# Optimization experiments

Hardware: AMD Instinct MI355X
Metric: run time of the kernel (lower is better)

## Reference

```python
import jax, jax.numpy as jnp
import numpy as np

E = 1024   # embed_dim
H = 16     # num_heads
D = E // H # head_dim = 64
P = 32     # project_dim
BS = 32768


def setup_inputs() -> dict:
    key0 = jax.random.key(0)
    ks = jax.random.split(key0, 16)
    s = 0.02
    inp = {
        "query": jax.random.normal(ks[0], (BS, E), jnp.float32),
        "key": jax.random.normal(ks[1], (BS, E), jnp.float32),
        "value": jax.random.normal(ks[2], (BS, E), jnp.float32),
        "attn_bias": jax.random.normal(ks[3], (BS, H), jnp.float32),
        # q/k/v embedding linears: [E, H*D]
        "Wq": jax.random.normal(ks[4], (E, H * D), jnp.float32) * s,
        "bq": jnp.zeros((H * D,), jnp.float32),
        "Wk": jax.random.normal(ks[5], (E, H * D), jnp.float32) * s,
        "bk": jnp.zeros((H * D,), jnp.float32),
        "Wv": jax.random.normal(ks[6], (E, H * D), jnp.float32) * s,
        "bv": jnp.zeros((H * D,), jnp.float32),
        # key/value low-rank projection linears: [E, H*P]
        "We": jax.random.normal(ks[7], (E, H * P), jnp.float32) * s,
        "be": jnp.zeros((H * P,), jnp.float32),
        "Wf": jax.random.normal(ks[8], (E, H * P), jnp.float32) * s,
        "bf": jnp.zeros((H * P,), jnp.float32),
        # feature_expand: [H, H*P]
        "Wfe": jax.random.normal(ks[9], (H, H * P), jnp.float32) * s,
        "bfe": jnp.zeros((H * P,), jnp.float32),
        # out_linear: [H*D, E]
        "Wo": jax.random.normal(ks[10], (H * D, E), jnp.float32) * s,
        "bo": jnp.zeros((E,), jnp.float32),
    }
    return inp


def reference(query, key, value, attn_bias,
              Wq, bq, Wk, bk, Wv, bv,
              We, be, Wf, bf, Wfe, bfe, Wo, bo):
    bs = query.shape[0]
    scale = 1.0 / np.sqrt(D).astype(np.float32)

    q = (query @ Wq + bq).reshape(bs, H, D)   # [bs, H, D]
    k = (key @ Wk + bk).reshape(bs, H, D)     # [bs, H, D]
    v = (value @ Wv + bv).reshape(bs, H, D)   # [bs, H, D]
    e = (key @ We + be).reshape(bs, H, P)     # [bs, H, P]
    f = (value @ Wf + bf).reshape(bs, H, P)   # [bs, H, P]

    # With tgt_len=src_len=1: q @ (e @ k)^T == (q.k) * e  (outer-product collapse)
    qk = jnp.einsum('bhd,bhd->bh', q, k)                     # [bs, H]
    bias = (attn_bias @ Wfe + bfe).reshape(bs, H, P)          # [bs, H, P]
    attn = scale * qk[..., None] * e + bias                   # [bs, H, P]
    attn = jax.nn.softmax(attn, axis=-1)                      # dropout p=0 (eval)

    # attn @ (f @ v) == (attn.f) * v
    af = jnp.einsum('bhp,bhp->bh', attn, f)                   # [bs, H]
    out = (af[..., None] * v).reshape(bs, H * D) @ Wo + bo    # [bs, E]
    return out
```

## Files before the change

### kernel.cpp

```cpp
#include <hip/hip_runtime.h>
#include <hip/hip_bf16.h>
#include <stdint.h>

#define BS_N 32768
#define E_DIM 1024

typedef __bf16 bf16x8 __attribute__((ext_vector_type(8)));
typedef float f32x4 __attribute__((ext_vector_type(4)));

__device__ __forceinline__ float asf(uint32_t u){ union{uint32_t u;float f;}x; x.u=u; return x.f; }
__device__ __forceinline__ uint32_t asu(float f){ union{float f;uint32_t u;}x; x.f=f; return x.u; }
__device__ __forceinline__ float blo(uint32_t u){ return asf(u<<16); }
__device__ __forceinline__ float bhi(uint32_t u){ return asf(u & 0xffff0000u); }
__device__ __forceinline__ uint16_t f2b(float f){
  uint32_t u = asu(f);
  u = u + 0x7fffu + ((u>>16)&1u);
  return (uint16_t)(u>>16);
}
__device__ __forceinline__ uint32_t pack2(float lo, float hi){
  return (uint32_t)f2b(lo) | ((uint32_t)f2b(hi)<<16);
}

#define GLD16(g, l) __builtin_amdgcn_global_load_lds( \
    (__attribute__((address_space(1))) const void*)(g), \
    (__attribute__((address_space(3))) void*)(l), 16, 0, 0)

#define BAR() __builtin_amdgcn_s_barrier()
#define LGKM0() do{ asm volatile("s_waitcnt lgkmcnt(0)" ::: "memory"); __builtin_amdgcn_sched_barrier(0); }while(0)
#define VMC8() do{ asm volatile("s_waitcnt vmcnt(8)" ::: "memory"); __builtin_amdgcn_sched_barrier(0); }while(0)
#define VMC0() do{ asm volatile("s_waitcnt vmcnt(0)" ::: "memory"); __builtin_amdgcn_sched_barrier(0); }while(0)

__global__ __launch_bounds__(256) void cast3(const float4* __restrict__ q,
                                             const float4* __restrict__ k,
                                             const float4* __restrict__ v,
                                             uint2* __restrict__ oq,
                                             uint2* __restrict__ ok,
                                             uint2* __restrict__ ov){
  const int n4 = (BS_N*E_DIM)/4;
  int i = blockIdx.x*256 + threadIdx.x;
  int stride = gridDim.x*256;
  for (; i < 3*n4; i += stride){
    int seg = i >> 23;
    int j = i & (n4 - 1);
    const float4* in = seg==0 ? q : (seg==1 ? k : v);
    uint2* out = seg==0 ? oq : (seg==1 ? ok : ov);
    float4 w = in[j];
    uint2 o; o.x = pack2(w.x, w.y); o.y = pack2(w.z, w.w);
    out[j] = o;
  }
}

__global__ __launch_bounds__(256) void transpose_cast(const float* __restrict__ W,
                                                      uint16_t* __restrict__ WT,
                                                      int R, int C){
  __shared__ float tile[32][33];
  int c0 = blockIdx.x*32, r0 = blockIdx.y*32;
  int tx = threadIdx.x, ty = threadIdx.y;
  #pragma unroll
  for (int i=0;i<32;i+=8) tile[ty+i][tx] = W[(size_t)(r0+ty+i)*C + c0+tx];
  __syncthreads();
  #pragma unroll
  for (int i=0;i<32;i+=8) WT[(size_t)(c0+ty+i)*R + r0+tx] = f2b(tile[tx][ty+i]);
}

__global__ __launch_bounds__(256) void prep_ab(const float* __restrict__ ab,
                                               uint16_t* __restrict__ abp){
  int i = blockIdx.x*256 + threadIdx.x;
  int b = i >> 5, j = i & 31;
  abp[i] = f2b(j < 16 ? ab[b*16 + j] : 0.f);
}

__global__ __launch_bounds__(256) void prep_wfe(const float* __restrict__ Wfe,
                                                uint16_t* __restrict__ WfeTp){
  int i = blockIdx.x*256 + threadIdx.x;
  int n = i >> 5, j = i & 31;
  float v = (j < 16) ? Wfe[j*512 + n] : 0.f;
  WfeTp[n*32 + j] = f2b(v);
}

__global__ __launch_bounds__(256) void cat2(const float* __restrict__ a, int na,
                                            const float* __restrict__ b, int nb,
                                            float* __restrict__ o){
  int i = blockIdx.x*256 + threadIdx.x;
  if (i < na) o[i] = a[i];
  else if (i < na + nb) o[i] = b[i - na];
}

template<int BF16OUT>
__device__ __forceinline__ void g256_body(const uint16_t* __restrict__ A,
                                          const uint16_t* __restrict__ BT,
                                          const float* __restrict__ bias,
                                          void* __restrict__ Cp,
                                          int N, int K, int row0, int col0,
                                          char* ldsA, char* ldsB){
  const int tid  = threadIdx.x;
  const int lane = tid & 63;
  const int w    = tid >> 6;
  const int wm   = w >> 2;
  const int wn   = w & 3;
  const int r    = lane & 15;
  const int kc   = lane >> 4;

  f32x4 acc[8][4];
  #pragma unroll
  for (int i=0;i<8;i++)
    #pragma unroll
    for (int j=0;j<4;j++){ f32x4 z = {0.f,0.f,0.f,0.f}; acc[i][j] = z; }

  const int NT = K >> 6;
  const size_t K2 = (size_t)K * 2;

  const int sr  = tid >> 3;
  const int scS = ((tid & 7) << 4) ^ ((sr & 7) << 4);
  const char* gA = (const char*)(A  + (size_t)row0 * K) + (size_t)sr*K2 + scS;
  const char* gB = (const char*)(BT + (size_t)col0 * K) + (size_t)sr*K2 + scS;

  #define STAGE_A(b, hh, u) do{ \
    const char* s_ = gA + (size_t)(hh)*(K2<<7) + ((size_t)(u)<<7); \
    char* d_ = ldsA + ((b)<<15) + ((hh)<<14) + (tid<<4); \
    GLD16(s_, d_); GLD16(s_ + (K2<<6), d_ + 8192); }while(0)
  #define STAGE_B(b, hh, u) do{ \
    const char* s_ = gB + (size_t)(hh)*(K2<<7) + ((size_t)(u)<<7); \
    char* d_ = ldsB + ((b)<<15) + ((hh)<<14) + (tid<<4); \
    GLD16(s_, d_); GLD16(s_ + (K2<<6), d_ + 8192); }while(0)

  const int rdKey = (kc << 4) ^ ((r & 7) << 4);
  const char* aR = ldsA + ((wm*128 + r) * 128);
  const char* bR = ldsB + ((wn*64  + r) * 128);

  bf16x8 afr[4][2], bf0[2][2], bf1[2][2];

  #define READ_A(QM) do{ \
    _Pragma("unroll") for (int fm=0; fm<4; ++fm) \
    _Pragma("unroll") for (int ks=0; ks<2; ++ks) \
      afr[fm][ks] = *(const bf16x8*)(aB + (QM)*8192 + fm*2048 + (rdKey ^ (ks<<6))); }while(0)
  #define READ_B(DST, QN) do{ \
    _Pragma("unroll") for (int fn=0; fn<2; ++fn) \
    _Pragma("unroll") for (int ks=0; ks<2; ++ks) \
      DST[fn][ks] = *(const bf16x8*)(bB + (QN)*4096 + fn*2048 + (rdKey ^ (ks<<6))); }while(0)
  #define MFMA16(QM, QN, BF) do{ \
    __builtin_amdgcn_s_setprio(1); \
    _Pragma("unroll") for (int ks=0; ks<2; ++ks) \
    _Pragma("unroll") for (int fm=0; fm<4; ++fm) \
    _Pragma("unroll") for (int fn=0; fn<2; ++fn) \
      acc[(QM)*4+fm][(QN)*2+fn] = __builtin_amdgcn_mfma_f32_16x16x32_bf16( \
        afr[fm][ks], BF[fn][ks], acc[(QM)*4+fm][(QN)*2+fn], 0, 0, 0); \
    __builtin_amdgcn_s_setprio(0); }while(0)

  STAGE_A(0,0,0); STAGE_B(0,0,0); STAGE_B(0,1,0); STAGE_A(0,1,0);
  if (NT > 1){ STAGE_A(1,0,1); STAGE_B(1,0,1); STAGE_B(1,1,1); STAGE_A(1,1,1); VMC8(); }
  else       { VMC0(); }
  BAR();

  for (int t = 0; t < NT; ++t){
    const int buf = t & 1;
    const char* aB = aR + (buf << 15);
    const char* bB = bR + (buf << 15);
    READ_A(0); READ_B(bf0, 0);
    BAR(); LGKM0();
    MFMA16(0,0,bf0);
    BAR();
    READ_B(bf1, 1);
    BAR(); LGKM0();
    MFMA16(0,1,bf1);
    BAR();
    READ_A(1);
    if (t+2 < NT){ STAGE_B(buf, 0, t+2); STAGE_B(buf, 1, t+2); }
    BAR(); LGKM0();
    MFMA16(1,0,bf0);
    BAR();
    if (t+2 < NT){ STAGE_A(buf, 0, t+2); STAGE_A(buf, 1, t+2); }
    BAR(); LGKM0();
    MFMA16(1,1,bf1);
    if (t+2 < NT) { VMC8(); } else { VMC0(); }
    BAR();
  }

  const int crow = row0 + wm*128 + ((lane>>4)<<2);
  const int ccol = col0 + wn*64 + (lane & 15);
  #pragma unroll
  for (int i=0;i<8;i++){
    #pragma unroll
    for (int n=0;n<4;n++){
      int col = ccol + n*16;
      float bv = bias[col];
      #pragma unroll
      for (int j=0;j<4;j++){
        float val = acc[i][n][j] + bv;
        int row = crow + i*16 + j;
        if (BF16OUT) __builtin_nontemporal_store(f2b(val), ((uint16_t*)Cp) + (size_t)row*N + col);
        else         __builtin_nontemporal_store(val,      ((float*)Cp)    + (size_t)row*N + col);
      }
    }
  }
  #undef STAGE_A
  #undef STAGE_B
  #undef READ_A
  #undef READ_B
  #undef MFMA16
}

template<int BF16OUT>
__global__ __launch_bounds__(512, 2) void gemm256s(const uint16_t* __restrict__ A,
                                                   const uint16_t* __restrict__ BT,
                                                   const float* __restrict__ bias,
                                                   void* __restrict__ Cp,
                                                   int N, int K){
  __shared__ alignas(16) uint16_t As_[2][16384];
  __shared__ alignas(16) uint16_t Bs_[2][16384];
  int bid = (int)blockIdx.x;
  int nwg = (int)gridDim.x;
  int cpx = nwg >> 3;
  int swz = (bid & 7)*cpx + (bid >> 3);
  const int rowTile = swz & 127;
  const int colTile = swz >> 7;
  g256_body<BF16OUT>(A, BT, bias, Cp, N, K, rowTile<<8, colTile<<8,
                     (char*)&As_[0][0], (char*)&Bs_[0][0]);
}

__global__ __launch_bounds__(512, 2) void gemm256g(
    const uint16_t* __restrict__ A0, const uint16_t* __restrict__ A1, const uint16_t* __restrict__ A2,
    const uint16_t* __restrict__ B0, const uint16_t* __restrict__ B1, const uint16_t* __restrict__ B2,
    const float* __restrict__ f0, const float* __restrict__ f1, const float* __restrict__ f2,
    uint16_t* __restrict__ C0, uint16_t* __restrict__ C1, uint16_t* __restrict__ C2,
    int n0, int n1, int n2, int ct1, int ct2, int K){
  __shared__ alignas(16) uint16_t As_[2][16384];
  __shared__ alignas(16) uint16_t Bs_[2][16384];
  int bid = (int)blockIdx.x;
  int nwg = (int)gridDim.x;
  int cpx = nwg >> 3;
  int swz = (bid & 7)*cpx + (bid >> 3);
  const int rowTile = swz & 127;
  const int colTile = swz >> 7;

  const uint16_t* A; const uint16_t* BT; const float* bias; uint16_t* C; int N; int ctl;
  if (colTile < ct1)      { A=A0; BT=B0; bias=f0; C=C0; N=n0; ctl=colTile; }
  else if (colTile < ct2) { A=A1; BT=B1; bias=f1; C=C1; N=n1; ctl=colTile-ct1; }
  else                    { A=A2; BT=B2; bias=f2; C=C2; N=n2; ctl=colTile-ct2; }
  g256_body<1>(A, BT, bias, C, N, K, rowTile<<8, ctl<<8,
               (char*)&As_[0][0], (char*)&Bs_[0][0]);
}

template<int BF16OUT>
__global__ __launch_bounds__(256) void gemm_bt(const uint16_t* __restrict__ A,
                                               const uint16_t* __restrict__ BT,
                                               const float* __restrict__ bias,
                                               void* __restrict__ Cp,
                                               int N, int K){
  __shared__ alignas(16) uint16_t As[128*32];
  __shared__ alignas(16) uint16_t Bs[128*32];
  const int tid  = threadIdx.x;
  const int lane = tid & 63;
  const int w    = tid >> 6;
  const int wr   = w >> 1, wc = w & 1;

  int bid = (int)blockIdx.x;
  int nwg = (int)gridDim.x;
  int cpx = nwg >> 3;
  int swz = (bid & 7)*cpx + (bid >> 3);
  int rowTile = swz & 255;
  int colTile = swz >> 8;
  const size_t row0 = (size_t)rowTile << 7;
  const int col0 = colTile << 7;

  f32x4 acc[4][4];
  #pragma unroll
  for (int m=0;m<4;m++)
    #pragma unroll
    for (int n=0;n<4;n++){ f32x4 z = {0.f,0.f,0.f,0.f}; acc[m][n] = z; }

  const int c0 = tid, c1 = tid + 256;
  const int ar0 = c0 >> 2, ao0 = (c0 & 3) << 4;
  const int ar1 = c1 >> 2, ao1 = (c1 & 3) << 4;
  const size_t K2 = (size_t)K * 2;
  const char* Ab = (const char*)(A  + row0 * (size_t)K);
  const char* Bb = (const char*)(BT + (size_t)col0 * (size_t)K);
  const char* gA0 = Ab + (size_t)ar0*K2 + ao0;
  const char* gA1 = Ab + (size_t)ar1*K2 + ao1;
  const char* gB0 = Bb + (size_t)ar0*K2 + ao0;
  const char* gB1 = Bb + (size_t)ar1*K2 + ao1;
  char* lA0 = (char*)As + c0*16;
  char* lA1 = (char*)As + c1*16;
  char* lB0 = (char*)Bs + c0*16;
  char* lB1 = (char*)Bs + c1*16;

  const int r = lane & 15, kc = lane >> 4;
  const char* aRd = (const char*)As + ((wr<<6) + r)*64 + (kc<<4);
  const char* bRd = (const char*)Bs + ((wc<<6) + r)*64 + (kc<<4);

  for (int kt = 0; kt < K; kt += 32){
    GLD16(gA0 + kt*2, lA0);
    GLD16(gA1 + kt*2, lA1);
    GLD16(gB0 + kt*2, lB0);
    GLD16(gB1 + kt*2, lB1);
    __syncthreads();
    bf16x8 a[4], b[4];
    #pragma unroll
    for (int m=0;m<4;m++) a[m] = *(const bf16x8*)(aRd + m*1024);
    #pragma unroll
    for (int n=0;n<4;n++) b[n] = *(const bf16x8*)(bRd + n*1024);
    #pragma unroll
    for (int m=0;m<4;m++)
      #pragma unroll
      for (int n=0;n<4;n++)
        acc[m][n] = __builtin_amdgcn_mfma_f32_16x16x32_bf16(a[m], b[n], acc[m][n], 0, 0, 0);
    __syncthreads();
  }

  const int crow = (int)row0 + (wr<<6) + ((lane>>4)<<2);
  const int ccol = col0 + (wc<<6) + (lane & 15);
  #pragma unroll
  for (int n=0;n<4;n++){
    int col = ccol + n*16;
    float bv = bias[col];
    #pragma unroll
    for (int m=0;m<4;m++){
      #pragma unroll
      for (int j=0;j<4;j++){
        float val = acc[m][n][j] + bv;
        if (BF16OUT) ((uint16_t*)Cp)[(size_t)(crow + m*16 + j)*N + col] = f2b(val);
        else         ((float*)Cp)   [(size_t)(crow + m*16 + j)*N + col] = val;
      }
    }
  }
}

__global__ __launch_bounds__(256) void middle(const uint16_t* __restrict__ qo,
                                              const uint16_t* __restrict__ keo,
                                              const uint16_t* __restrict__ vfo,
                                              const uint16_t* __restrict__ bb,
                                              uint16_t* __restrict__ t){
  int tid = blockIdx.x*256 + threadIdx.x;
  int b = tid >> 4, h = tid & 15;

  const uint4* qp = (const uint4*)(qo  + ((size_t)b<<10) + (h<<6));
  const uint4* kp = (const uint4*)(keo + (size_t)b*1536 + (h<<6));
  float qk = 0.f;
  #pragma unroll
  for (int i=0;i<8;i++){
    uint4 x = qp[i], y = kp[i];
    qk += blo(x.x)*blo(y.x) + bhi(x.x)*bhi(y.x);
    qk += blo(x.y)*blo(y.y) + bhi(x.y)*bhi(y.y);
    qk += blo(x.z)*blo(y.z) + bhi(x.z)*bhi(y.z);
    qk += blo(x.w)*blo(y.w) + bhi(x.w)*bhi(y.w);
  }
  qk *= 0.125f;

  const uint4* ep = (const uint4*)(keo + (size_t)b*1536 + 1024 + (h<<5));
  const uint4* bp = (const uint4*)(bb  + ((size_t)b<<9) + (h<<5));
  float s[32];
  #pragma unroll
  for (int i=0;i<4;i++){
    uint4 ev = ep[i], bv = bp[i];
    s[i*8+0] = qk*blo(ev.x) + blo(bv.x);
    s[i*8+1] = qk*bhi(ev.x) + bhi(bv.x);
    s[i*8+2] = qk*blo(ev.y) + blo(bv.y);
    s[i*8+3] = qk*bhi(ev.y) + bhi(bv.y);
    s[i*8+4] = qk*blo(ev.z) + blo(bv.z);
    s[i*8+5] = qk*bhi(ev.z) + bhi(bv.z);
    s[i*8+6] = qk*blo(ev.w) + blo(bv.w);
    s[i*8+7] = qk*bhi(ev.w) + bhi(bv.w);
  }
  float mx = s[0];
  #pragma unroll
  for (int p=1;p<32;p++) mx = fmaxf(mx, s[p]);
  float sum = 0.f;
  #pragma unroll
  for (int p=0;p<32;p++){ s[p] = __expf(s[p]-mx); sum += s[p]; }

  const uint4* fp = (const uint4*)(vfo + (size_t)b*1536 + 1024 + (h<<5));
  float af = 0.f;
  #pragma unroll
  for (int i=0;i<4;i++){
    uint4 fv = fp[i];
    af += s[i*8+0]*blo(fv.x) + s[i*8+1]*bhi(fv.x);
    af += s[i*8+2]*blo(fv.y) + s[i*8+3]*bhi(fv.y);
    af += s[i*8+4]*blo(fv.z) + s[i*8+5]*bhi(fv.z);
    af += s[i*8+6]*blo(fv.w) + s[i*8+7]*bhi(fv.w);
  }
  af /= sum;

  const uint4* vp = (const uint4*)(vfo + (size_t)b*1536 + (h<<6));
  uint4* tp = (uint4*)(t + ((size_t)b<<10) + (h<<6));
  #pragma unroll
  for (int i=0;i<8;i++){
    uint4 vv = vp[i];
    uint4 o;
    o.x = pack2(af*blo(vv.x), af*bhi(vv.x));
    o.y = pack2(af*blo(vv.y), af*bhi(vv.y));
    o.z = pack2(af*blo(vv.z), af*bhi(vv.z));
    o.w = pack2(af*blo(vv.w), af*bhi(vv.w));
    tp[i] = o;
  }
}

extern "C" void kernel_launch(void* const* d_in, const int* in_sizes, int n_in,
                              void* d_out, int out_size, void* d_ws, size_t ws_size,
                              hipStream_t stream){
  const float* query = (const float*)d_in[0];
  const float* key   = (const float*)d_in[1];
  const float* value = (const float*)d_in[2];
  const float* ab    = (const float*)d_in[3];
  const float* Wq  = (const float*)d_in[4];
  const float* bq  = (const float*)d_in[5];
  const float* Wk  = (const float*)d_in[6];
  const float* bk  = (const float*)d_in[7];
  const float* Wv  = (const float*)d_in[8];
  const float* bv  = (const float*)d_in[9];
  const float* We  = (const float*)d_in[10];
  const float* be  = (const float*)d_in[11];
  const float* Wf  = (const float*)d_in[12];
  const float* bfp = (const float*)d_in[13];
  const float* Wfe = (const float*)d_in[14];
  const float* bfe = (const float*)d_in[15];
  const float* Wo  = (const float*)d_in[16];
  const float* bo  = (const float*)d_in[17];

  char* ws = (char*)d_ws;
  const size_t MB = (size_t)1 << 20;
  uint16_t* kb    = (uint16_t*)(ws +   0*MB);
  uint16_t* vb    = (uint16_t*)(ws +  64*MB);
  uint16_t* qb    = (uint16_t*)(ws + 128*MB);
  uint16_t* qo    = (uint16_t*)(ws + 192*MB);
  uint16_t* keo   = (uint16_t*)(ws + 256*MB);
  uint16_t* vfo   = (uint16_t*)(ws + 352*MB);
  uint16_t* bb    = (uint16_t*)(ws + 448*MB);
  uint16_t* abp   = (uint16_t*)(ws + 480*MB);
  uint16_t* WqT   = (uint16_t*)(ws + 482*MB);
  uint16_t* WkeT  = (uint16_t*)(ws + 484*MB);
  uint16_t* WvfT  = (uint16_t*)(ws + 487*MB);
  uint16_t* WoT   = (uint16_t*)(ws + 490*MB);
  uint16_t* WfeTp = (uint16_t*)(ws + 492*MB);
  float*    bke   = (float*)   (ws + 493*MB);
  float*    bvf   = (float*)   (ws + 493*MB + 16384);
  uint16_t* t     = qb;

  cast3<<<3072,256,0,stream>>>((const float4*)query, (const float4*)key, (const float4*)value,
                               (uint2*)qb, (uint2*)kb, (uint2*)vb);

  dim3 tb(32,8);
  transpose_cast<<<dim3(32,32),tb,0,stream>>>(Wq, WqT, 1024, 1024);
  transpose_cast<<<dim3(32,32),tb,0,stream>>>(Wk, WkeT, 1024, 1024);
  transpose_cast<<<dim3(16,32),tb,0,stream>>>(We, WkeT + (size_t)1024*1024, 1024, 512);
  transpose_cast<<<dim3(32,32),tb,0,stream>>>(Wv, WvfT, 1024, 1024);
  transpose_cast<<<dim3(16,32),tb,0,stream>>>(Wf, WvfT + (size_t)1024*1024, 1024, 512);
  transpose_cast<<<dim3(32,32),tb,0,stream>>>(Wo, WoT, 1024, 1024);
  prep_ab<<<4096,256,0,stream>>>(ab, abp);
  prep_wfe<<<64,256,0,stream>>>(Wfe, WfeTp);
  cat2<<<6,256,0,stream>>>(bk, 1024, be, 512, bke);
  cat2<<<6,256,0,stream>>>(bv, 1024, bfp, 512, bvf);

  gemm256g<<<2048,512,0,stream>>>(qb, kb, vb,
                                  WqT, WkeT, WvfT,
                                  bq, bke, bvf,
                                  qo, keo, vfo,
                                  1024, 1536, 1536, 4, 10, 1024);

  gemm_bt<1><<<1024,256,0,stream>>>(abp, WfeTp, bfe, bb, 512, 32);

  middle<<<2048,256,0,stream>>>(qo, keo, vfo, bb, t);

  gemm256s<0><<<512,512,0,stream>>>(t, WoT, bo, d_out, 1024, 1024);
}
```

Measured before the change: 1.010 ms.

## Fuse attn-bias feature-expand into middle kernel and merge weight transposes

The small attn_bias @ Wfe GEMM, its prep kernels and the bf16 bias buffer are removed. The middle kernel now computes the 32 bias values per (batch, head) directly in fp32 from attn_bias, Wfe and bfe, which avoids writing and re-reading a 32 MB intermediate. Six transpose launches are merged into one kernel that dispatches on block index. GEMM epilogue stores also drop the nontemporal hint. The cost is extra per-thread FMAs and redundant Wfe loads in middle, which should mostly hit cache.

```diff
diff --git a/kernel.cpp b/kernel.cpp
--- a/kernel.cpp
+++ b/kernel.cpp
@@ -50,32 +50,31 @@
   }
 }
 
-__global__ __launch_bounds__(256) void transpose_cast(const float* __restrict__ W,
-                                                      uint16_t* __restrict__ WT,
-                                                      int R, int C){
+__global__ __launch_bounds__(256) void transpose_all(
+    const float* __restrict__ Wq, const float* __restrict__ Wk,
+    const float* __restrict__ We, const float* __restrict__ Wv,
+    const float* __restrict__ Wf, const float* __restrict__ Wo,
+    uint16_t* __restrict__ WqT, uint16_t* __restrict__ WkeT,
+    uint16_t* __restrict__ WvfT, uint16_t* __restrict__ WoT){
   __shared__ float tile[32][33];
-  int c0 = blockIdx.x*32, r0 = blockIdx.y*32;
-  int tx = threadIdx.x, ty = threadIdx.y;
+  int bid = (int)blockIdx.x;
+  const float* W; uint16_t* WT; int C; int lb;
+  if (bid < 1024)      { W=Wq; WT=WqT;                        C=1024; lb=bid; }
+  else if (bid < 2048) { W=Wk; WT=WkeT;                       C=1024; lb=bid-1024; }
+  else if (bid < 2560) { W=We; WT=WkeT+(size_t)1024*1024;     C=512;  lb=bid-2048; }
+  else if (bid < 3584) { W=Wv; WT=WvfT;                       C=1024; lb=bid-2560; }
+  else if (bid < 4096) { W=Wf; WT=WvfT+(size_t)1024*1024;     C=512;  lb=bid-3584; }
+  else                 { W=Wo; WT=WoT;                        C=1024; lb=bid-4096; }
+  const int ctm = (C >> 5) - 1;
+  const int shs = (C == 1024) ? 5 : 4;
+  int bx = lb & ctm, by = lb >> shs;
+  int c0 = bx*32, r0 = by*32;
+  int tx = threadIdx.x & 31, ty = threadIdx.x >> 5;
   #pragma unroll
   for (int i=0;i<32;i+=8) tile[ty+i][tx] = W[(size_t)(r0+ty+i)*C + c0+tx];
   __syncthreads();
   #pragma unroll
-  for (int i=0;i<32;i+=8) WT[(size_t)(c0+ty+i)*R + r0+tx] = f2b(tile[tx][ty+i]);
-}
-
-__global__ __launch_bounds__(256) void prep_ab(const float* __restrict__ ab,
-                                               uint16_t* __restrict__ abp){
-  int i = blockIdx.x*256 + threadIdx.x;
-  int b = i >> 5, j = i & 31;
-  abp[i] = f2b(j < 16 ? ab[b*16 + j] : 0.f);
-}
-
-__global__ __launch_bounds__(256) void prep_wfe(const float* __restrict__ Wfe,
-                                                uint16_t* __restrict__ WfeTp){
-  int i = blockIdx.x*256 + threadIdx.x;
-  int n = i >> 5, j = i & 31;
-  float v = (j < 16) ? Wfe[j*512 + n] : 0.f;
-  WfeTp[n*32 + j] = f2b(v);
+  for (int i=0;i<32;i+=8) WT[(size_t)(c0+ty+i)*1024 + r0+tx] = f2b(tile[tx][ty+i]);
 }
 
 __global__ __launch_bounds__(256) void cat2(const float* __restrict__ a, int na,
@@ -188,8 +187,8 @@
       for (int j=0;j<4;j++){
         float val = acc[i][n][j] + bv;
         int row = crow + i*16 + j;
-        if (BF16OUT) __builtin_nontemporal_store(f2b(val), ((uint16_t*)Cp) + (size_t)row*N + col);
-        else         __builtin_nontemporal_store(val,      ((float*)Cp)    + (size_t)row*N + col);
+        if (BF16OUT) ((uint16_t*)Cp)[(size_t)row*N + col] = f2b(val);
+        else         ((float*)Cp)   [(size_t)row*N + col] = val;
       }
     }
   }
@@ -241,94 +240,12 @@
                (char*)&As_[0][0], (char*)&Bs_[0][0]);
 }
 
-template<int BF16OUT>
-__global__ __launch_bounds__(256) void gemm_bt(const uint16_t* __restrict__ A,
-                                               const uint16_t* __restrict__ BT,
-                                               const float* __restrict__ bias,
-                                               void* __restrict__ Cp,
-                                               int N, int K){
-  __shared__ alignas(16) uint16_t As[128*32];
-  __shared__ alignas(16) uint16_t Bs[128*32];
-  const int tid  = threadIdx.x;
-  const int lane = tid & 63;
-  const int w    = tid >> 6;
-  const int wr   = w >> 1, wc = w & 1;
-
-  int bid = (int)blockIdx.x;
-  int nwg = (int)gridDim.x;
-  int cpx = nwg >> 3;
-  int swz = (bid & 7)*cpx + (bid >> 3);
-  int rowTile = swz & 255;
-  int colTile = swz >> 8;
-  const size_t row0 = (size_t)rowTile << 7;
-  const int col0 = colTile << 7;
-
-  f32x4 acc[4][4];
-  #pragma unroll
-  for (int m=0;m<4;m++)
-    #pragma unroll
-    for (int n=0;n<4;n++){ f32x4 z = {0.f,0.f,0.f,0.f}; acc[m][n] = z; }
-
-  const int c0 = tid, c1 = tid + 256;
-  const int ar0 = c0 >> 2, ao0 = (c0 & 3) << 4;
-  const int ar1 = c1 >> 2, ao1 = (c1 & 3) << 4;
-  const size_t K2 = (size_t)K * 2;
-  const char* Ab = (const char*)(A  + row0 * (size_t)K);
-  const char* Bb = (const char*)(BT + (size_t)col0 * (size_t)K);
-  const char* gA0 = Ab + (size_t)ar0*K2 + ao0;
-  const char* gA1 = Ab + (size_t)ar1*K2 + ao1;
-  const char* gB0 = Bb + (size_t)ar0*K2 + ao0;
-  const char* gB1 = Bb + (size_t)ar1*K2 + ao1;
-  char* lA0 = (char*)As + c0*16;
-  char* lA1 = (char*)As + c1*16;
-  char* lB0 = (char*)Bs + c0*16;
-  char* lB1 = (char*)Bs + c1*16;
-
-  const int r = lane & 15, kc = lane >> 4;
-  const char* aRd = (const char*)As + ((wr<<6) + r)*64 + (kc<<4);
-  const char* bRd = (const char*)Bs + ((wc<<6) + r)*64 + (kc<<4);
-
-  for (int kt = 0; kt < K; kt += 32){
-    GLD16(gA0 + kt*2, lA0);
-    GLD16(gA1 + kt*2, lA1);
-    GLD16(gB0 + kt*2, lB0);
-    GLD16(gB1 + kt*2, lB1);
-    __syncthreads();
-    bf16x8 a[4], b[4];
-    #pragma unroll
-    for (int m=0;m<4;m++) a[m] = *(const bf16x8*)(aRd + m*1024);
-    #pragma unroll
-    for (int n=0;n<4;n++) b[n] = *(const bf16x8*)(bRd + n*1024);
-    #pragma unroll
-    for (int m=0;m<4;m++)
-      #pragma unroll
-      for (int n=0;n<4;n++)
-        acc[m][n] = __builtin_amdgcn_mfma_f32_16x16x32_bf16(a[m], b[n], acc[m][n], 0, 0, 0);
-    __syncthreads();
-  }
-
-  const int crow = (int)row0 + (wr<<6) + ((lane>>4)<<2);
-  const int ccol = col0 + (wc<<6) + (lane & 15);
-  #pragma unroll
-  for (int n=0;n<4;n++){
-    int col = ccol + n*16;
-    float bv = bias[col];
-    #pragma unroll
-    for (int m=0;m<4;m++){
-      #pragma unroll
-      for (int j=0;j<4;j++){
-        float val = acc[m][n][j] + bv;
-        if (BF16OUT) ((uint16_t*)Cp)[(size_t)(crow + m*16 + j)*N + col] = f2b(val);
-        else         ((float*)Cp)   [(size_t)(crow + m*16 + j)*N + col] = val;
-      }
-    }
-  }
-}
-
 __global__ __launch_bounds__(256) void middle(const uint16_t* __restrict__ qo,
                                               const uint16_t* __restrict__ keo,
                                               const uint16_t* __restrict__ vfo,
-                                              const uint16_t* __restrict__ bb,
+                                              const float* __restrict__ ab,
+                                              const float* __restrict__ Wfe,
+                                              const float* __restrict__ bfe,
                                               uint16_t* __restrict__ t){
   int tid = blockIdx.x*256 + threadIdx.x;
   int b = tid >> 4, h = tid & 15;
@@ -346,20 +263,44 @@
   }
   qk *= 0.125f;
 
+  float s[32];
+  const float4* bfp4 = (const float4*)(bfe + h*32);
+  #pragma unroll
+  for (int i=0;i<8;i++){
+    float4 z = bfp4[i];
+    s[i*4+0]=z.x; s[i*4+1]=z.y; s[i*4+2]=z.z; s[i*4+3]=z.w;
+  }
+  float a[16];
+  const float4* ap4 = (const float4*)(ab + b*16);
+  #pragma unroll
+  for (int i=0;i<4;i++){
+    float4 z = ap4[i];
+    a[i*4+0]=z.x; a[i*4+1]=z.y; a[i*4+2]=z.z; a[i*4+3]=z.w;
+  }
+  #pragma unroll
+  for (int j=0;j<16;j++){
+    const float4* wr = (const float4*)(Wfe + j*512 + h*32);
+    float aj = a[j];
+    #pragma unroll
+    for (int i=0;i<8;i++){
+      float4 wv = wr[i];
+      s[i*4+0] += aj*wv.x; s[i*4+1] += aj*wv.y;
+      s[i*4+2] += aj*wv.z; s[i*4+3] += aj*wv.w;
+    }
+  }
+
   const uint4* ep = (const uint4*)(keo + (size_t)b*1536 + 1024 + (h<<5));
-  const uint4* bp = (const uint4*)(bb  + ((size_t)b<<9) + (h<<5));
-  float s[32];
   #pragma unroll
   for (int i=0;i<4;i++){
-    uint4 ev = ep[i], bv = bp[i];
-    s[i*8+0] = qk*blo(ev.x) + blo(bv.x);
-    s[i*8+1] = qk*bhi(ev.x) + bhi(bv.x);
-    s[i*8+2] = qk*blo(ev.y) + blo(bv.y);
-    s[i*8+3] = qk*bhi(ev.y) + bhi(bv.y);
-    s[i*8+4] = qk*blo(ev.z) + blo(bv.z);
-    s[i*8+5] = qk*bhi(ev.z) + bhi(bv.z);
-    s[i*8+6] = qk*blo(ev.w) + blo(bv.w);
-    s[i*8+7] = qk*bhi(ev.w) + bhi(bv.w);
+    uint4 ev = ep[i];
+    s[i*8+0] = qk*blo(ev.x) + s[i*8+0];
+    s[i*8+1] = qk*bhi(ev.x) + s[i*8+1];
+    s[i*8+2] = qk*blo(ev.y) + s[i*8+2];
+    s[i*8+3] = qk*bhi(ev.y) + s[i*8+3];
+    s[i*8+4] = qk*blo(ev.z) + s[i*8+4];
+    s[i*8+5] = qk*bhi(ev.z) + s[i*8+5];
+    s[i*8+6] = qk*blo(ev.w) + s[i*8+6];
+    s[i*8+7] = qk*bhi(ev.w) + s[i*8+7];
   }
   float mx = s[0];
   #pragma unroll
@@ -424,13 +365,10 @@
   uint16_t* qo    = (uint16_t*)(ws + 192*MB);
   uint16_t* keo   = (uint16_t*)(ws + 256*MB);
   uint16_t* vfo   = (uint16_t*)(ws + 352*MB);
-  uint16_t* bb    = (uint16_t*)(ws + 448*MB);
-  uint16_t* abp   = (uint16_t*)(ws + 480*MB);
   uint16_t* WqT   = (uint16_t*)(ws + 482*MB);
   uint16_t* WkeT  = (uint16_t*)(ws + 484*MB);
   uint16_t* WvfT  = (uint16_t*)(ws + 487*MB);
   uint16_t* WoT   = (uint16_t*)(ws + 490*MB);
-  uint16_t* WfeTp = (uint16_t*)(ws + 492*MB);
   float*    bke   = (float*)   (ws + 493*MB);
   float*    bvf   = (float*)   (ws + 493*MB + 16384);
   uint16_t* t     = qb;
@@ -438,15 +376,8 @@
   cast3<<<3072,256,0,stream>>>((const float4*)query, (const float4*)key, (const float4*)value,
                                (uint2*)qb, (uint2*)kb, (uint2*)vb);
 
-  dim3 tb(32,8);
-  transpose_cast<<<dim3(32,32),tb,0,stream>>>(Wq, WqT, 1024, 1024);
-  transpose_cast<<<dim3(32,32),tb,0,stream>>>(Wk, WkeT, 1024, 1024);
-  transpose_cast<<<dim3(16,32),tb,0,stream>>>(We, WkeT + (size_t)1024*1024, 1024, 512);
-  transpose_cast<<<dim3(32,32),tb,0,stream>>>(Wv, WvfT, 1024, 1024);
-  transpose_cast<<<dim3(16,32),tb,0,stream>>>(Wf, WvfT + (size_t)1024*1024, 1024, 512);
-  transpose_cast<<<dim3(32,32),tb,0,stream>>>(Wo, WoT, 1024, 1024);
-  prep_ab<<<4096,256,0,stream>>>(ab, abp);
-  prep_wfe<<<64,256,0,stream>>>(Wfe, WfeTp);
+  transpose_all<<<5120,256,0,stream>>>(Wq, Wk, We, Wv, Wf, Wo,
+                                       WqT, WkeT, WvfT, WoT);
   cat2<<<6,256,0,stream>>>(bk, 1024, be, 512, bke);
   cat2<<<6,256,0,stream>>>(bv, 1024, bfp, 512, bvf);
 
@@ -456,9 +387,7 @@
                                   qo, keo, vfo,
                                   1024, 1536, 1536, 4, 10, 1024);
 
-  gemm_bt<1><<<1024,256,0,stream>>>(abp, WfeTp, bfe, bb, 512, 32);
-
-  middle<<<2048,256,0,stream>>>(qo, keo, vfo, bb, t);
+  middle<<<2048,256,0,stream>>>(qo, keo, vfo, ab, Wfe, bfe, t);
 
   gemm256s<0><<<512,512,0,stream>>>(t, WoT, bo, d_out, 1024, 1024);
 }
```

Result: slower. 1.048 ms (+3.8%).
